# Kernel tuning notes

Hardware: AMD Instinct MI355X
Metric: run time of the kernel (lower is better)

## Reference

```python
import jax, jax.numpy as jnp
import numpy as np

DROPOUT_P = 0.3


def setup_inputs() -> dict:
    key = jax.random.key(0)
    kq, kk, kv, ks = jax.random.split(key, 4)
    B, Sq, Skv, D = 32, 2048, 2048, 128
    q = jax.random.normal(kq, (B, Sq, D), dtype=jnp.float32)
    k = jax.random.normal(kk, (B, Skv, D), dtype=jnp.float32)
    v = jax.random.normal(kv, (B, Skv, D), dtype=jnp.float32)
    # torch.randint(low=1, high=256, size=[B,1]) -> per-batch positive scale
    scale_factor = jax.random.randint(ks, (B, 1, 1), 1, 256).astype(jnp.float32)
    return {"q": q, "k": k, "v": v, "scale_factor": scale_factor}


def reference(q, k, v, scale_factor):
    # qk = q @ k^T ; div by scale_factor**-1 == multiply by scale_factor
    scores = jnp.einsum("bqd,bkd->bqk", q, k) * scale_factor  # [B,Sq,Skv]
    attn = jax.nn.softmax(scores, axis=-1)
    # dropout with fixed key (deterministic reference for torch F.dropout)
    keep_p = 1.0 - DROPOUT_P
    dk = jax.random.key(42)
    keep = jax.random.bernoulli(dk, keep_p, attn.shape)
    attn_d = jnp.where(keep, attn / keep_p, 0.0)
    return jnp.einsum("bqk,bkd->bqd", attn_d, v)
```

## Files before the change

kernel.cpp:

```cpp
#include <hip/hip_runtime.h>
#include <stdint.h>


namespace {

constexpr int Bb  = 32;
constexpr int SQ  = 2048;
constexpr int SKV = 2048;
constexpr int DH  = 128;
constexpr int KT  = 32;
constexpr int NKT = SKV / KT;
constexpr int TILE_F16 = 12288;
constexpr size_t WS_NEED = (size_t)Bb * NKT * TILE_F16 * 2;
constexpr int PSTR = KT + 8;

typedef _Float16 f16x8 __attribute__((ext_vector_type(8)));
typedef _Float16 f16x4 __attribute__((ext_vector_type(4)));
typedef float    f32x4 __attribute__((ext_vector_type(4)));

__device__ __forceinline__ uint32_t rotl32(uint32_t x, int d) {
  return (x << d) | (x >> (32 - d));
}

__device__ __forceinline__ uint32_t jax_random_bits(uint32_t i) {
  constexpr uint32_t K0 = 0u;
  constexpr uint32_t K1 = 42u;
  constexpr uint32_t K2 = 0x1BD11BDAu ^ K0 ^ K1;
  uint32_t x0 = K0;
  uint32_t x1 = i + K1;
#define TF4(a,b,c,d) \
  x0 += x1; x1 = rotl32(x1,a); x1 ^= x0; \
  x0 += x1; x1 = rotl32(x1,b); x1 ^= x0; \
  x0 += x1; x1 = rotl32(x1,c); x1 ^= x0; \
  x0 += x1; x1 = rotl32(x1,d); x1 ^= x0;
  TF4(13,15,26,6)   x0 += K1; x1 += K2 + 1u;
  TF4(17,29,16,24)  x0 += K2; x1 += K0 + 2u;
  TF4(13,15,26,6)   x0 += K0; x1 += K1 + 3u;
  TF4(17,29,16,24)  x0 += K1; x1 += K2 + 4u;
  TF4(13,15,26,6)   x0 += K2; x1 += K0 + 5u;
#undef TF4
  return x0 ^ x1;
}

__device__ __forceinline__ bool jax_keep(uint32_t i) {
  const uint32_t fb = (jax_random_bits(i) >> 9) | 0x3f800000u;
  return (__uint_as_float(fb) - 1.0f) < 0.7f;
}

__device__ __forceinline__ _Float16 hi16(float x) { return (_Float16)x; }
__device__ __forceinline__ _Float16 lo16(float x) {
  return (_Float16)(x - (float)((_Float16)x));
}

}

__global__ __launch_bounds__(256) void prep_tile(const float* __restrict__ Kg,
                                                 const float* __restrict__ Vg,
                                                 _Float16* __restrict__ ws) {
  __shared__ alignas(16) float sT[KT][DH + 4];

  const int tid  = threadIdx.x;
  const int b    = blockIdx.x >> 6;
  const int kt   = blockIdx.x & 63;
  _Float16* tile = ws + (size_t)(b * NKT + kt) * TILE_F16;

  {
    const float* kb = Kg + ((size_t)b * SKV + kt * KT) * DH;
#pragma unroll
    for (int rep = 0; rep < 4; ++rep) {
      const int idx = tid + 256 * rep;
      const int row = idx >> 5;
      const int c4  = idx & 31;
      *reinterpret_cast<float4*>(&sT[row][4 * c4]) =
          *reinterpret_cast<const float4*>(kb + (size_t)row * DH + 4 * c4);
    }
  }
  __syncthreads();
#pragma unroll
  for (int rep = 0; rep < 2; ++rep) {
    const int task = tid + 256 * rep;
    const int lane = task & 63;
    const int f    = task >> 6;
    const int ks   = f >> 1;
    const int ct   = f & 1;
    const int cl   = lane & 15;
    const int g8   = (lane >> 4) * 8;
    const float* src = &sT[ct * 16 + cl][ks * 32 + g8];
    f16x8 h, l;
#pragma unroll
    for (int j = 0; j < 8; ++j) { h[j] = hi16(src[j]); l[j] = lo16(src[j]); }
    *reinterpret_cast<f16x8*>(tile + f * 512 + lane * 8)        = h;
    *reinterpret_cast<f16x8*>(tile + 4096 + f * 512 + lane * 8) = l;
  }
  __syncthreads();

  {
    const float* vb = Vg + ((size_t)b * SKV + kt * KT) * DH;
#pragma unroll
    for (int rep = 0; rep < 4; ++rep) {
      const int idx = tid + 256 * rep;
      const int row = idx >> 5;
      const int c4  = idx & 31;
      *reinterpret_cast<float4*>(&sT[row][4 * c4]) =
          *reinterpret_cast<const float4*>(vb + (size_t)row * DH + 4 * c4);
    }
  }
  __syncthreads();
#pragma unroll
  for (int rep = 0; rep < 2; ++rep) {
    const int task = tid + 256 * rep;
    const int lane = task & 63;
    const int dt   = task >> 6;
    const int cl   = lane & 15;
    const int g8   = (lane >> 4) * 8;
    f16x8 w;
#pragma unroll
    for (int j = 0; j < 8; ++j)
      w[j] = (_Float16)sT[g8 + j][dt * 16 + cl];
    *reinterpret_cast<f16x8*>(tile + 8192 + dt * 512 + lane * 8) = w;
  }
}

__global__ __launch_bounds__(256, 3) void fused_attn5(
    const float* __restrict__ Qg, const _Float16* __restrict__ Wk,
    const float* __restrict__ Sg, float* __restrict__ Og)
{
  __shared__ alignas(16) _Float16 sStage[TILE_F16];
  __shared__ alignas(16) _Float16 sP[4][16][PSTR];

  const int tid  = threadIdx.x;
  const int wid  = tid >> 6;
  const int lane = tid & 63;
  const int cl   = lane & 15;
  const int g8   = (lane >> 4) * 8;
  const int r0   = (lane >> 4) * 4;

  const int logical = (blockIdx.x & 7) * 128 + (blockIdx.x >> 3);
  const int b  = logical >> 5;
  const int q0 = (logical & 31) * 64;
  const float scale = Sg[b];

  f16x8 qhi[4], qlo[4];
  {
    const float* qp = Qg + ((size_t)b * SQ + q0 + wid * 16 + cl) * DH + g8;
#pragma unroll
    for (int ks = 0; ks < 4; ++ks) {
      const float4 a0 = *reinterpret_cast<const float4*>(qp + 32 * ks);
      const float4 a1 = *reinterpret_cast<const float4*>(qp + 32 * ks + 4);
      const float xs[8] = {a0.x, a0.y, a0.z, a0.w, a1.x, a1.y, a1.z, a1.w};
#pragma unroll
      for (int j = 0; j < 8; ++j) { qhi[ks][j] = hi16(xs[j]); qlo[ks][j] = lo16(xs[j]); }
    }
  }

  float m_run[4], l_run[4], alpha[4];
  f32x4 oacc[8];
#pragma unroll
  for (int i = 0; i < 4; ++i) { m_run[i] = -INFINITY; l_run[i] = 0.0f; }
#pragma unroll
  for (int dt = 0; dt < 8; ++dt) oacc[dt] = (f32x4){0.f, 0.f, 0.f, 0.f};

  for (int kt = 0; kt < NKT; ++kt) {
    __syncthreads();

    const uint32_t* tsrc =
        reinterpret_cast<const uint32_t*>(Wk + (size_t)(b * NKT + kt) * TILE_F16);
#pragma unroll
    for (int c = 0; c < 6; ++c) {
      const int j = wid + 4 * c;
      __builtin_amdgcn_global_load_lds(tsrc + j * 256 + lane * 4,
          reinterpret_cast<uint32_t*>(&sStage[j * 512]), 16, 0, 0);
    }
    __syncthreads();

    f32x4 sacc[2];
    __builtin_amdgcn_s_setprio(1);
#pragma unroll
    for (int ct = 0; ct < 2; ++ct) {
      sacc[ct] = (f32x4){0.f, 0.f, 0.f, 0.f};
#pragma unroll
      for (int ks = 0; ks < 4; ++ks) {
        const int f = ks * 2 + ct;
        const f16x8 bhi = *reinterpret_cast<const f16x8*>(&sStage[f * 512 + lane * 8]);
        const f16x8 blo = *reinterpret_cast<const f16x8*>(&sStage[4096 + f * 512 + lane * 8]);
        sacc[ct] = __builtin_amdgcn_mfma_f32_16x16x32_f16(qhi[ks], bhi, sacc[ct], 0, 0, 0);
        sacc[ct] = __builtin_amdgcn_mfma_f32_16x16x32_f16(qlo[ks], bhi, sacc[ct], 0, 0, 0);
        sacc[ct] = __builtin_amdgcn_mfma_f32_16x16x32_f16(qhi[ks], blo, sacc[ct], 0, 0, 0);
      }
    }
    __builtin_amdgcn_s_setprio(0);

    bool anyalpha = false;
    bool tk[4];
#pragma unroll
    for (int i = 0; i < 4; ++i) {
      float mraw = fmaxf(sacc[0][i], sacc[1][i]);
#pragma unroll
      for (int off = 8; off >= 1; off >>= 1)
        mraw = fmaxf(mraw, __shfl_xor(mraw, off, 64));
      const float mt = mraw * scale;

      tk[i] = (mt >= m_run[i] - 9.21f);
      if (tk[i]) {
        const float mnew = fmaxf(m_run[i], mt);
        alpha[i] = __expf(m_run[i] - mnew);
        m_run[i] = mnew;
        const int qrow = q0 + wid * 16 + r0 + i;
        const uint32_t rowbase =
            ((uint32_t)b * (uint32_t)SQ + (uint32_t)qrow) * (uint32_t)SKV
            + (uint32_t)(kt * KT);
        float ps = 0.0f;
#pragma unroll
        for (int ct = 0; ct < 2; ++ct) {
          const float p = __expf(sacc[ct][i] * scale - mnew);
          ps += p;
          const bool keep = jax_keep(rowbase + (uint32_t)(16 * ct + cl));
          sP[wid][r0 + i][16 * ct + cl] = keep ? (_Float16)(p * (1.0f / 0.7f))
                                               : (_Float16)0.0f;
        }
#pragma unroll
        for (int off = 8; off >= 1; off >>= 1)
          ps += __shfl_xor(ps, off, 64);
        l_run[i] = l_run[i] * alpha[i] + ps;
        anyalpha |= (alpha[i] != 1.0f);
      } else {
        alpha[i] = 1.0f;
      }
    }

    const int myAllSkip = !(tk[0] || tk[1] || tk[2] || tk[3]);
    if (!__all(myAllSkip)) {
#pragma unroll
      for (int i = 0; i < 4; ++i) {
        if (!tk[i]) {
#pragma unroll
          for (int ct = 0; ct < 2; ++ct)
            sP[wid][r0 + i][16 * ct + cl] = (_Float16)0.0f;
        }
      }

      if (anyalpha) {
#pragma unroll
        for (int dt = 0; dt < 8; ++dt)
#pragma unroll
          for (int i = 0; i < 4; ++i) oacc[dt][i] *= alpha[i];
      }

      const f16x8 pa = *reinterpret_cast<const f16x8*>(&sP[wid][cl][g8]);
      __builtin_amdgcn_s_setprio(1);
#pragma unroll
      for (int dt = 0; dt < 8; ++dt) {
        const f16x8 bv = *reinterpret_cast<const f16x8*>(
            &sStage[8192 + dt * 512 + lane * 8]);
        oacc[dt] = __builtin_amdgcn_mfma_f32_16x16x32_f16(pa, bv, oacc[dt], 0, 0, 0);
      }
      __builtin_amdgcn_s_setprio(0);
    }
  }

#pragma unroll
  for (int i = 0; i < 4; ++i) {
    const float inv_l = 1.0f / l_run[i];
    float* op = Og + ((size_t)b * SQ + (size_t)(q0 + wid * 16 + r0 + i)) * DH + cl;
#pragma unroll
    for (int dt = 0; dt < 8; ++dt)
      op[16 * dt] = oacc[dt][i] * inv_l;
  }
}

namespace {
constexpr int FKT  = 64;
constexpr int KSTR = DH + 8;
constexpr int VSTR = FKT + 8;
constexpr int FPSTR = FKT + 8;
}

__global__ __launch_bounds__(256, 2) void fused_attn_fb(
    const float* __restrict__ Qg, const float* __restrict__ Kg,
    const float* __restrict__ Vg, const float* __restrict__ Sg,
    float* __restrict__ Og)
{
  __shared__ alignas(16) _Float16 sKhi[FKT][KSTR];
  __shared__ alignas(16) _Float16 sKlo[FKT][KSTR];
  __shared__ alignas(16) _Float16 sVt[DH][VSTR];
  __shared__ alignas(16) _Float16 sP[4][16][FPSTR];

  const int tid  = threadIdx.x;
  const int wid  = tid >> 6;
  const int lane = tid & 63;
  const int cl   = lane & 15;
  const int g8   = (lane >> 4) * 8;
  const int r0   = (lane >> 4) * 4;

  const int b  = blockIdx.x >> 5;
  const int q0 = (blockIdx.x & 31) * 64;
  const float scale = Sg[b];

  f16x8 qhi[4], qlo[4];
  {
    const float* qp = Qg + ((size_t)b * SQ + q0 + wid * 16 + cl) * DH + g8;
#pragma unroll
    for (int ks = 0; ks < 4; ++ks) {
      const float4 a0 = *reinterpret_cast<const float4*>(qp + 32 * ks);
      const float4 a1 = *reinterpret_cast<const float4*>(qp + 32 * ks + 4);
      const float xs[8] = {a0.x, a0.y, a0.z, a0.w, a1.x, a1.y, a1.z, a1.w};
#pragma unroll
      for (int j = 0; j < 8; ++j) { qhi[ks][j] = hi16(xs[j]); qlo[ks][j] = lo16(xs[j]); }
    }
  }

  float m_run[4], l_run[4], alpha[4];
  f32x4 oacc[8];
#pragma unroll
  for (int i = 0; i < 4; ++i) { m_run[i] = -INFINITY; l_run[i] = 0.0f; }
#pragma unroll
  for (int dt = 0; dt < 8; ++dt) oacc[dt] = (f32x4){0.f, 0.f, 0.f, 0.f};

  for (int k0 = 0; k0 < SKV; k0 += FKT) {
    __syncthreads();
#pragma unroll
    for (int rep = 0; rep < 8; ++rep) {
      const int idx = tid + 256 * rep;
      const int row = idx >> 5;
      const int c4  = idx & 31;
      const float4 t = *reinterpret_cast<const float4*>(
          Kg + ((size_t)b * SKV + k0 + row) * DH + 4 * c4);
      f16x4 h4, l4;
      h4[0] = hi16(t.x); l4[0] = lo16(t.x);
      h4[1] = hi16(t.y); l4[1] = lo16(t.y);
      h4[2] = hi16(t.z); l4[2] = lo16(t.z);
      h4[3] = hi16(t.w); l4[3] = lo16(t.w);
      *reinterpret_cast<f16x4*>(&sKhi[row][4 * c4]) = h4;
      *reinterpret_cast<f16x4*>(&sKlo[row][4 * c4]) = l4;
    }
#pragma unroll
    for (int rep = 0; rep < 2; ++rep) {
      const int u  = tid + 256 * rep;
      const int du = u & 31;
      const int ku = u >> 5;
      const float* vb = Vg + ((size_t)b * SKV + k0 + 4 * ku) * DH + 4 * du;
      float4 t[4];
#pragma unroll
      for (int j = 0; j < 4; ++j)
        t[j] = *reinterpret_cast<const float4*>(vb + (size_t)j * DH);
#pragma unroll
      for (int dd = 0; dd < 4; ++dd) {
        const float v0 = (&t[0].x)[dd], v1 = (&t[1].x)[dd],
                    v2 = (&t[2].x)[dd], v3 = (&t[3].x)[dd];
        f16x4 w4 = {(_Float16)v0, (_Float16)v1, (_Float16)v2, (_Float16)v3};
        *reinterpret_cast<f16x4*>(&sVt[4 * du + dd][4 * ku]) = w4;
      }
    }
    __syncthreads();

    f32x4 sacc[4];
#pragma unroll
    for (int ct = 0; ct < 4; ++ct) {
      sacc[ct] = (f32x4){0.f, 0.f, 0.f, 0.f};
#pragma unroll
      for (int ks = 0; ks < 4; ++ks) {
        const f16x8 bhi = *reinterpret_cast<const f16x8*>(&sKhi[16 * ct + cl][32 * ks + g8]);
        const f16x8 blo = *reinterpret_cast<const f16x8*>(&sKlo[16 * ct + cl][32 * ks + g8]);
        sacc[ct] = __builtin_amdgcn_mfma_f32_16x16x32_f16(qhi[ks], bhi, sacc[ct], 0, 0, 0);
        sacc[ct] = __builtin_amdgcn_mfma_f32_16x16x32_f16(qlo[ks], bhi, sacc[ct], 0, 0, 0);
        sacc[ct] = __builtin_amdgcn_mfma_f32_16x16x32_f16(qhi[ks], blo, sacc[ct], 0, 0, 0);
      }
    }

    bool anyalpha = false;
#pragma unroll
    for (int i = 0; i < 4; ++i) {
      float mraw = fmaxf(fmaxf(sacc[0][i], sacc[1][i]), fmaxf(sacc[2][i], sacc[3][i]));
#pragma unroll
      for (int off = 8; off >= 1; off >>= 1)
        mraw = fmaxf(mraw, __shfl_xor(mraw, off, 64));
      const float mt = mraw * scale;
      if (mt >= m_run[i] - 9.21f) {
        const float mnew = fmaxf(m_run[i], mt);
        alpha[i] = __expf(m_run[i] - mnew);
        m_run[i] = mnew;
        const int qrow = q0 + wid * 16 + r0 + i;
        const uint32_t rowbase =
            ((uint32_t)b * (uint32_t)SQ + (uint32_t)qrow) * (uint32_t)SKV + (uint32_t)k0;
        float ps = 0.0f;
#pragma unroll
        for (int ct = 0; ct < 4; ++ct) {
          const float p = __expf(sacc[ct][i] * scale - mnew);
          ps += p;
          const bool keep = jax_keep(rowbase + (uint32_t)(16 * ct + cl));
          sP[wid][r0 + i][16 * ct + cl] = keep ? (_Float16)(p * (1.0f / 0.7f))
                                               : (_Float16)0.0f;
        }
#pragma unroll
        for (int off = 8; off >= 1; off >>= 1)
          ps += __shfl_xor(ps, off, 64);
        l_run[i] = l_run[i] * alpha[i] + ps;
        anyalpha |= (alpha[i] != 1.0f);
      } else {
        alpha[i] = 1.0f;
#pragma unroll
        for (int ct = 0; ct < 4; ++ct)
          sP[wid][r0 + i][16 * ct + cl] = (_Float16)0.0f;
      }
    }

    if (anyalpha) {
#pragma unroll
      for (int dt = 0; dt < 8; ++dt)
#pragma unroll
        for (int i = 0; i < 4; ++i) oacc[dt][i] *= alpha[i];
    }
#pragma unroll
    for (int ks2 = 0; ks2 < 2; ++ks2) {
      const f16x8 pa = *reinterpret_cast<const f16x8*>(&sP[wid][cl][32 * ks2 + g8]);
#pragma unroll
      for (int dt = 0; dt < 8; ++dt) {
        const f16x8 bv = *reinterpret_cast<const f16x8*>(&sVt[16 * dt + cl][32 * ks2 + g8]);
        oacc[dt] = __builtin_amdgcn_mfma_f32_16x16x32_f16(pa, bv, oacc[dt], 0, 0, 0);
      }
    }
  }

#pragma unroll
  for (int i = 0; i < 4; ++i) {
    const float inv_l = 1.0f / l_run[i];
    float* op = Og + ((size_t)b * SQ + (size_t)(q0 + wid * 16 + r0 + i)) * DH + cl;
#pragma unroll
    for (int dt = 0; dt < 8; ++dt)
      op[16 * dt] = oacc[dt][i] * inv_l;
  }
}

extern "C" void kernel_launch(void* const* d_in, const int* in_sizes, int n_in,
                              void* d_out, int out_size, void* d_ws, size_t ws_size,
                              hipStream_t stream) {
  (void)in_sizes; (void)n_in; (void)out_size;
  const float* q  = (const float*)d_in[0];
  const float* k  = (const float*)d_in[1];
  const float* v  = (const float*)d_in[2];
  const float* sc = (const float*)d_in[3];
  float* out = (float*)d_out;

  if (ws_size >= WS_NEED) {
    _Float16* ws = (_Float16*)d_ws;
    prep_tile<<<dim3(Bb * NKT), dim3(256), 0, stream>>>(k, v, ws);
    fused_attn5<<<dim3(Bb * (SQ / 64)), dim3(256), 0, stream>>>(q, ws, sc, out);
  } else {
    fused_attn_fb<<<dim3(Bb * (SQ / 64)), dim3(256), 0, stream>>>(q, k, v, sc, out);
  }
}
```

Baseline: 389.7 us.

## Skip dropout RNG for negligible probabilities and simplify keep test

Replaces the float-based keep test with an integer threshold compare on the random bits. In the first loop, the Threefry hash is skipped whenever no lane in the wave has an exponent argument above a cutoff, since those probabilities would flush to zero in fp16 anyway. It also drops the XCD-aware block remapping in favour of a linear block-to-tile mapping. The RNG is a large share of per-element ALU work, so skipping it cuts compute. The trade-offs are possible loss of L2 locality from the new block mapping and tiny numerical differences for values near the cutoff.

```diff
diff --git a/kernel.cpp b/kernel.cpp
--- a/kernel.cpp
+++ b/kernel.cpp
@@ -42,9 +42,8 @@
   return x0 ^ x1;
 }
 
-__device__ __forceinline__ bool jax_keep(uint32_t i) {
-  const uint32_t fb = (jax_random_bits(i) >> 9) | 0x3f800000u;
-  return (__uint_as_float(fb) - 1.0f) < 0.7f;
+__device__ __forceinline__ bool jax_keep_bits(uint32_t bits) {
+  return (bits >> 9) < 0x0059999Au;
 }
 
 __device__ __forceinline__ _Float16 hi16(float x) { return (_Float16)x; }
@@ -135,9 +134,8 @@
   const int g8   = (lane >> 4) * 8;
   const int r0   = (lane >> 4) * 4;
 
-  const int logical = (blockIdx.x & 7) * 128 + (blockIdx.x >> 3);
-  const int b  = logical >> 5;
-  const int q0 = (logical & 31) * 64;
+  const int b  = blockIdx.x >> 5;
+  const int q0 = (blockIdx.x & 31) * 64;
   const float scale = Sg[b];
 
   f16x8 qhi[4], qlo[4];
@@ -209,20 +207,34 @@
         const uint32_t rowbase =
             ((uint32_t)b * (uint32_t)SQ + (uint32_t)qrow) * (uint32_t)SKV
             + (uint32_t)(kt * KT);
-        float ps = 0.0f;
-#pragma unroll
-        for (int ct = 0; ct < 2; ++ct) {
-          const float p = __expf(sacc[ct][i] * scale - mnew);
-          ps += p;
-          const bool keep = jax_keep(rowbase + (uint32_t)(16 * ct + cl));
-          sP[wid][r0 + i][16 * ct + cl] = keep ? (_Float16)(p * (1.0f / 0.7f))
-                                               : (_Float16)0.0f;
-        }
+
+        const float t0 = sacc[0][i] * scale - mnew;
+        const float t1 = sacc[1][i] * scale - mnew;
+        const float p0 = __expf(t0);
+        const float p1 = __expf(t1);
+        float ps = p0 + p1;
 #pragma unroll
         for (int off = 8; off >= 1; off >>= 1)
           ps += __shfl_xor(ps, off, 64);
         l_run[i] = l_run[i] * alpha[i] + ps;
         anyalpha |= (alpha[i] != 1.0f);
+
+        if (__any(t0 >= -17.75f)) {
+          const uint32_t bits = jax_random_bits(rowbase + (uint32_t)cl);
+          sP[wid][r0 + i][cl] = jax_keep_bits(bits)
+                                    ? (_Float16)(p0 * (1.0f / 0.7f))
+                                    : (_Float16)0.0f;
+        } else {
+          sP[wid][r0 + i][cl] = (_Float16)0.0f;
+        }
+        if (__any(t1 >= -17.75f)) {
+          const uint32_t bits = jax_random_bits(rowbase + (uint32_t)(16 + cl));
+          sP[wid][r0 + i][16 + cl] = jax_keep_bits(bits)
+                                         ? (_Float16)(p1 * (1.0f / 0.7f))
+                                         : (_Float16)0.0f;
+        } else {
+          sP[wid][r0 + i][16 + cl] = (_Float16)0.0f;
+        }
       } else {
         alpha[i] = 1.0f;
       }
@@ -387,7 +399,7 @@
         for (int ct = 0; ct < 4; ++ct) {
           const float p = __expf(sacc[ct][i] * scale - mnew);
           ps += p;
-          const bool keep = jax_keep(rowbase + (uint32_t)(16 * ct + cl));
+          const bool keep = jax_keep_bits(jax_random_bits(rowbase + (uint32_t)(16 * ct + cl)));
           sP[wid][r0 + i][16 * ct + cl] = keep ? (_Float16)(p * (1.0f / 0.7f))
                                                : (_Float16)0.0f;
         }
```

Result: faster. 353.9 us (-9.2%).
